# Kernel tuning notes

Hardware: AMD Instinct MI355X
Metric: run time of the kernel (lower is better)

## Reference

```python
import math
import jax, jax.numpy as jnp
import numpy as np

H = 8
C_HIDDEN = 32
C_Q = 256


def setup_inputs() -> dict:
    key = jax.random.key(0)
    ks = jax.random.split(key, 9)
    B, S, Q, K = 1, 128, 256, 256
    q_x = jax.random.normal(ks[0], (B, S, Q, C_Q), dtype=jnp.float32)
    kv_x = jax.random.normal(ks[1], (B, S, K, C_Q), dtype=jnp.float32)
    bias1 = jax.random.normal(ks[2], (B, S, 1, 1, K), dtype=jnp.float32)
    bias2 = jax.random.normal(ks[3], (B, 1, H, Q, K), dtype=jnp.float32)
    scale = 1.0 / math.sqrt(C_Q)
    wq = jax.random.normal(ks[4], (H * C_HIDDEN, C_Q), dtype=jnp.float32) * scale
    wk = jax.random.normal(ks[5], (H * C_HIDDEN, C_Q), dtype=jnp.float32) * scale
    wv = jax.random.normal(ks[6], (H * C_HIDDEN, C_Q), dtype=jnp.float32) * scale
    wg = jax.random.normal(ks[7], (H * C_HIDDEN, C_Q), dtype=jnp.float32) * scale
    wo = jax.random.normal(ks[8], (C_Q, H * C_HIDDEN), dtype=jnp.float32) * scale
    return {"q_x": q_x, "kv_x": kv_x, "bias1": bias1, "bias2": bias2,
            "wq": wq, "wk": wk, "wv": wv, "wg": wg, "wo": wo}


def _split_heads(x):
    # [..., L, H*c] -> [..., H, L, c]
    y = x.reshape(x.shape[:-1] + (H, C_HIDDEN))
    return jnp.moveaxis(y, -2, -3)


def reference(q_x, kv_x, bias1, bias2, wq, wk, wv, wg, wo):
    # QKV projections (no bias), per-head split, scale q by 1/sqrt(c_hidden)
    q = _split_heads(q_x @ wq.T) / math.sqrt(C_HIDDEN)   # [B,S,H,Q,c]
    k = _split_heads(kv_x @ wk.T)                         # [B,S,H,K,c]
    v = _split_heads(kv_x @ wv.T)                         # [B,S,H,K,c]
    # attention logits with additive biases folded in
    a = jnp.einsum('...hqc,...hkc->...hqk', q, k) + bias1 + bias2
    a = jax.nn.softmax(a, axis=-1)
    o = jnp.einsum('...hqk,...hkc->...hqc', a, v)         # [B,S,H,Q,c]
    o = jnp.moveaxis(o, -3, -2)                           # [B,S,Q,H,c]
    # sigmoid gating from query data
    g = jax.nn.sigmoid(q_x @ wg.T)                        # [B,S,Q,H*c]
    g = g.reshape(g.shape[:-1] + (H, C_HIDDEN))
    o = o * g
    o = o.reshape(o.shape[:-2] + (H * C_HIDDEN,))         # flatten heads
    return o @ wo.T                                       # [B,S,Q,C_Q]
```

## Files before the change

kernel.cpp:

```cpp
#include <hip/hip_runtime.h>
#include <math.h>

#define S_DIM 128
#define H_DIM 8
#define M_TOT (S_DIM * 256)

typedef unsigned short ushort_t;
typedef unsigned int   uint32;
typedef __bf16  v8bf  __attribute__((ext_vector_type(8)));
typedef float   v4f   __attribute__((ext_vector_type(4)));

__device__ inline ushort_t f2b(float x) {
    unsigned int u = __float_as_uint(x);
    u += 0x7fffu + ((u >> 16) & 1u);
    return (ushort_t)(u >> 16);
}
__device__ inline float b2f(ushort_t h) {
    return __uint_as_float(((unsigned int)h) << 16);
}

#define GLDS16(gp, lp) __builtin_amdgcn_global_load_lds( \
    (const __attribute__((address_space(1))) void*)(gp), \
    (__attribute__((address_space(3))) void*)(lp), 16, 0, 0)

__global__ __launch_bounds__(256) void split_x(
    const float* __restrict__ xq, const float* __restrict__ xkv,
    ushort_t* __restrict__ hi, ushort_t* __restrict__ lo)
{
    const size_t BUF4 = (size_t)M_TOT * 64;
    const float* src = blockIdx.y ? xkv : xq;
    size_t base = (size_t)blockIdx.y * BUF4;
    int i = blockIdx.x * 256 + threadIdx.x;
    float4 v = ((const float4*)src)[i];
    ushort4 h, l;
    h.x = f2b(v.x); l.x = f2b(v.x - b2f(h.x));
    h.y = f2b(v.y); l.y = f2b(v.y - b2f(h.y));
    h.z = f2b(v.z); l.z = f2b(v.z - b2f(h.z));
    h.w = f2b(v.w); l.w = f2b(v.w - b2f(h.w));
    ((ushort4*)hi)[base + i] = h;
    ((ushort4*)lo)[base + i] = l;
}

__global__ __launch_bounds__(256) void split_w(
    const float* __restrict__ w0, const float* __restrict__ w1,
    const float* __restrict__ w2, const float* __restrict__ w3,
    const float* __restrict__ w4,
    ushort_t* __restrict__ hi, ushort_t* __restrict__ lo)
{
    const float* src;
    switch (blockIdx.y) {
        case 0: src = w0; break; case 1: src = w1; break;
        case 2: src = w2; break; case 3: src = w3; break;
        default: src = w4; break;
    }
    int i = blockIdx.x * 256 + threadIdx.x;
    float4 v = ((const float4*)src)[i];
    ushort4 h, l;
    h.x = f2b(v.x); l.x = f2b(v.x - b2f(h.x));
    h.y = f2b(v.y); l.y = f2b(v.y - b2f(h.y));
    h.z = f2b(v.z); l.z = f2b(v.z - b2f(h.z));
    h.w = f2b(v.w); l.w = f2b(v.w - b2f(h.w));
    size_t base = (size_t)blockIdx.y * 16384;
    ((ushort4*)hi)[base + i] = h;
    ((ushort4*)lo)[base + i] = l;
}


__global__ __launch_bounds__(256) void gemm_proj(
    const ushort_t* __restrict__ Xhi, const ushort_t* __restrict__ Xlo,
    const ushort_t* __restrict__ Whi4, const ushort_t* __restrict__ Wlo4,
    ushort_t* __restrict__ qh, ushort_t* __restrict__ ql,
    ushort_t* __restrict__ kh, ushort_t* __restrict__ kl,
    float* __restrict__ g_out,
    ushort_t* __restrict__ vh,
    float qscale)
{
    __shared__ ushort_t lds[4][128 * 32];

    const int z    = blockIdx.z;
    const int L    = blockIdx.x + 4 * blockIdx.y;
    const int mti  = ((L >> 5) << 3) + (L & 7);
    const int nti  = (L >> 3) & 3;
    const int t    = threadIdx.x;
    const int l    = t & 63;
    const int wv   = t >> 6;
    const int wm   = wv & 1;
    const int wn   = wv >> 1;
    const int idx  = l & 15;
    const int quad = l >> 4;
    const int m0   = mti * 128;
    const int n0   = nti * 128;

    const size_t BUF = (size_t)M_TOT * 256;
    const ushort_t* Ahi = Xhi + (size_t)z * BUF;
    const ushort_t* Alo = Xlo + (size_t)z * BUF;
    const ushort_t* Whi = Whi4 + (size_t)z * 131072;
    const ushort_t* Wlo = Wlo4 + (size_t)z * 131072;
    const float scale = z ? 1.f : qscale;

    const ushort_t* srcs[4] = { Ahi + (size_t)m0 * 256, Alo + (size_t)m0 * 256,
                                Whi + (size_t)n0 * 256, Wlo + (size_t)n0 * 256 };

    v4f acc[4][4];
    #pragma unroll
    for (int i = 0; i < 4; ++i)
        #pragma unroll
        for (int j = 0; j < 4; ++j) acc[i][j] = (v4f){0.f, 0.f, 0.f, 0.f};

    for (int k0 = 0; k0 < 256; k0 += 32) {
        #pragma unroll
        for (int b = 0; b < 4; ++b) {
            #pragma unroll
            for (int i = 0; i < 2; ++i) {
                const int sb   = wv * 128 + i * 64;
                const int slot = sb + l;
                const int row  = slot >> 2;
                const int gseg = ((slot & 3) - (row >> 1)) & 3;
                const ushort_t* g = srcs[b] + (size_t)row * 256 + k0 + gseg * 8;
                GLDS16(g, &lds[b][sb * 8]);
            }
        }
        __builtin_amdgcn_s_waitcnt(0);
        __syncthreads();

        v8bf ah[4], al[4], bh[4], bl[4];
        #pragma unroll
        for (int mt = 0; mt < 4; ++mt) {
            const int r   = wm * 64 + mt * 16 + idx;
            const int off = r * 32 + (((quad + (r >> 1)) & 3) << 3);
            ah[mt] = *(const v8bf*)&lds[0][off];
            al[mt] = *(const v8bf*)&lds[1][off];
        }
        #pragma unroll
        for (int nt = 0; nt < 4; ++nt) {
            const int r   = wn * 64 + nt * 16 + idx;
            const int off = r * 32 + (((quad + (r >> 1)) & 3) << 3);
            bh[nt] = *(const v8bf*)&lds[2][off];
            bl[nt] = *(const v8bf*)&lds[3][off];
        }

        #pragma unroll
        for (int mt = 0; mt < 4; ++mt)
            #pragma unroll
            for (int nt = 0; nt < 4; ++nt) {
                acc[mt][nt] = __builtin_amdgcn_mfma_f32_16x16x32_bf16(ah[mt], bh[nt], acc[mt][nt], 0, 0, 0);
                acc[mt][nt] = __builtin_amdgcn_mfma_f32_16x16x32_bf16(al[mt], bh[nt], acc[mt][nt], 0, 0, 0);
                acc[mt][nt] = __builtin_amdgcn_mfma_f32_16x16x32_bf16(ah[mt], bl[nt], acc[mt][nt], 0, 0, 0);
            }
        __syncthreads();
    }

    ushort_t* dsth = z ? kh : qh;
    ushort_t* dstl = z ? kl : ql;

    #pragma unroll
    for (int mt = 0; mt < 4; ++mt) {
        const int mbase = m0 + wm * 64 + mt * 16 + quad * 4;
        const int s = mbase >> 8, r8 = mbase & 255;
        #pragma unroll
        for (int nt = 0; nt < 4; ++nt) {
            const int gcol = n0 + wn * 64 + nt * 16 + idx;
            if (gcol < 256) {
                const int hh = gcol >> 5, c = gcol & 31;
                const size_t di = (((size_t)(s * 8 + hh) * 256) + r8) * 32 + c;
                #pragma unroll
                for (int r = 0; r < 4; ++r) {
                    const float val = acc[mt][nt][r] * scale;
                    const ushort_t hv = f2b(val);
                    dsth[di + (size_t)r * 32] = hv;
                    dstl[di + (size_t)r * 32] = f2b(val - b2f(hv));
                }
            } else if (z == 0) {
                const int gc = gcol - 256;
                #pragma unroll
                for (int r = 0; r < 4; ++r)
                    g_out[(size_t)(mbase + r) * 256 + gc] = acc[mt][nt][r];
            } else {
                const int gc = gcol - 256, hh = gc >> 5, c = gc & 31;
                ushort4 hv4;
                #pragma unroll
                for (int r = 0; r < 4; ++r)
                    ((ushort_t*)&hv4)[r] = f2b(acc[mt][nt][r]);
                const size_t di = (((size_t)(s * 8 + hh) * 32) + c) * 256 + r8;
                *(ushort4*)&vh[di] = hv4;
            }
        }
    }
}

__global__ __launch_bounds__(256) void gemm_out(
    const ushort_t* __restrict__ Ah, const ushort_t* __restrict__ Whi,
    const ushort_t* __restrict__ Wlo, float* __restrict__ Cf)
{
    __shared__ ushort_t lds[3][128 * 32];

    const int L    = blockIdx.x + 2 * blockIdx.y;
    const int mti  = ((L >> 4) << 3) + (L & 7);
    const int nti  = (L >> 3) & 1;
    const int t    = threadIdx.x;
    const int l    = t & 63;
    const int wv   = t >> 6;
    const int wm   = wv & 1;
    const int wn   = wv >> 1;
    const int idx  = l & 15;
    const int quad = l >> 4;
    const int m0   = mti * 128;
    const int n0   = nti * 128;

    const ushort_t* srcs[3] = { Ah + (size_t)m0 * 256,
                                Whi + (size_t)n0 * 256, Wlo + (size_t)n0 * 256 };

    v4f acc[4][4];
    #pragma unroll
    for (int i = 0; i < 4; ++i)
        #pragma unroll
        for (int j = 0; j < 4; ++j) acc[i][j] = (v4f){0.f, 0.f, 0.f, 0.f};

    for (int k0 = 0; k0 < 256; k0 += 32) {
        #pragma unroll
        for (int b = 0; b < 3; ++b) {
            #pragma unroll
            for (int i = 0; i < 2; ++i) {
                const int sb   = wv * 128 + i * 64;
                const int slot = sb + l;
                const int row  = slot >> 2;
                const int gseg = ((slot & 3) - (row >> 1)) & 3;
                const ushort_t* g = srcs[b] + (size_t)row * 256 + k0 + gseg * 8;
                GLDS16(g, &lds[b][sb * 8]);
            }
        }
        __builtin_amdgcn_s_waitcnt(0);
        __syncthreads();

        v8bf ah[4], bh[4], bl[4];
        #pragma unroll
        for (int mt = 0; mt < 4; ++mt) {
            const int r   = wm * 64 + mt * 16 + idx;
            const int off = r * 32 + (((quad + (r >> 1)) & 3) << 3);
            ah[mt] = *(const v8bf*)&lds[0][off];
        }
        #pragma unroll
        for (int nt = 0; nt < 4; ++nt) {
            const int r   = wn * 64 + nt * 16 + idx;
            const int off = r * 32 + (((quad + (r >> 1)) & 3) << 3);
            bh[nt] = *(const v8bf*)&lds[1][off];
            bl[nt] = *(const v8bf*)&lds[2][off];
        }

        #pragma unroll
        for (int mt = 0; mt < 4; ++mt)
            #pragma unroll
            for (int nt = 0; nt < 4; ++nt) {
                acc[mt][nt] = __builtin_amdgcn_mfma_f32_16x16x32_bf16(ah[mt], bh[nt], acc[mt][nt], 0, 0, 0);
                acc[mt][nt] = __builtin_amdgcn_mfma_f32_16x16x32_bf16(ah[mt], bl[nt], acc[mt][nt], 0, 0, 0);
            }
        __syncthreads();
    }

    #pragma unroll
    for (int mt = 0; mt < 4; ++mt) {
        #pragma unroll
        for (int nt = 0; nt < 4; ++nt) {
            const int gcol = n0 + wn * 64 + nt * 16 + idx;
            #pragma unroll
            for (int r = 0; r < 4; ++r) {
                const int grow = m0 + wm * 64 + mt * 16 + quad * 4 + r;
                Cf[(size_t)grow * 256 + gcol] = acc[mt][nt][r];
            }
        }
    }
}

__global__ __launch_bounds__(256, 2) void attn_mfma(
    const ushort_t* __restrict__ qh, const ushort_t* __restrict__ ql,
    const ushort_t* __restrict__ kh, const ushort_t* __restrict__ kl,
    const ushort_t* __restrict__ vth,
    const float* __restrict__ b1, const float* __restrict__ b2,
    const float* __restrict__ gbuf,
    ushort_t* __restrict__ oh)
{
    __shared__ __align__(16) uint32 pbuf[4][64 * 36];
    __shared__ __align__(16) float  invl[4][64];

    const int sh = blockIdx.x, s = sh >> 3, h = sh & 7;
    const int t = threadIdx.x, l = t & 63, w = t >> 6;
    const int idx = l & 15, quad = l >> 4;

    const size_t shb = (size_t)sh * 8192;
    const ushort_t* qhp = qh + shb;
    const ushort_t* qlp = ql + shb;
    const ushort_t* khp = kh + shb;
    const ushort_t* klp = kl + shb;
    const ushort_t* vhp = vth + shb;
    const float* b1p = b1 + (size_t)s * 256;
    const float* b2p = b2 + (size_t)h * 65536;

    v8bf qfh[4], qfl[4];
    #pragma unroll
    for (int nt = 0; nt < 4; ++nt) {
        const int off = (w * 64 + nt * 16 + idx) * 32 + quad * 8;
        qfh[nt] = *(const v8bf*)(qhp + off);
        qfl[nt] = *(const v8bf*)(qlp + off);
    }

    v4f oacc[4][2];
    #pragma unroll
    for (int mt = 0; mt < 4; ++mt) {
        oacc[mt][0] = (v4f){0.f, 0.f, 0.f, 0.f};
        oacc[mt][1] = (v4f){0.f, 0.f, 0.f, 0.f};
    }
    float lrun[4] = {0.f, 0.f, 0.f, 0.f};

    v8bf kbh[2][4], kbl[2][4];
    #pragma unroll
    for (int at = 0; at < 4; ++at) {
        const int off = (at * 16 + idx) * 32 + quad * 8;
        kbh[0][at] = *(const v8bf*)(khp + off);
        kbl[0][at] = *(const v8bf*)(klp + off);
    }

    #pragma unroll
    for (int c4 = 0; c4 < 4; ++c4) {
        const int ak0 = c4 * 64;
        const int cur = c4 & 1;

        if (c4 < 3) {
            #pragma unroll
            for (int at = 0; at < 4; ++at) {
                const int off = (ak0 + 64 + at * 16 + idx) * 32 + quad * 8;
                kbh[cur ^ 1][at] = *(const v8bf*)(khp + off);
                kbl[cur ^ 1][at] = *(const v8bf*)(klp + off);
            }
        }

        v8bf vfh[2][2];
        #pragma unroll
        for (int n2 = 0; n2 < 2; ++n2)
            #pragma unroll
            for (int kt = 0; kt < 2; ++kt) {
                const int off = (n2 * 16 + idx) * 256 + ak0 + kt * 32 + quad * 8;
                vfh[n2][kt] = *(const v8bf*)(vhp + off);
            }

        v4f sacc[4][4];
        #pragma unroll
        for (int at = 0; at < 4; ++at)
            #pragma unroll
            for (int nt = 0; nt < 4; ++nt)
                sacc[at][nt] = (v4f){0.f, 0.f, 0.f, 0.f};
        __builtin_amdgcn_s_setprio(1);
        #pragma unroll
        for (int at = 0; at < 4; ++at)
            #pragma unroll
            for (int nt = 0; nt < 4; ++nt) {
                sacc[at][nt] = __builtin_amdgcn_mfma_f32_16x16x32_bf16(kbh[cur][at], qfh[nt], sacc[at][nt], 0, 0, 0);
                sacc[at][nt] = __builtin_amdgcn_mfma_f32_16x16x32_bf16(kbl[cur][at], qfh[nt], sacc[at][nt], 0, 0, 0);
                sacc[at][nt] = __builtin_amdgcn_mfma_f32_16x16x32_bf16(kbh[cur][at], qfl[nt], sacc[at][nt], 0, 0, 0);
            }
        __builtin_amdgcn_s_setprio(0);

        v4f b1v[4];
        #pragma unroll
        for (int at = 0; at < 4; ++at)
            b1v[at] = *(const v4f*)(b1p + ak0 + at * 16 + quad * 4);

        #pragma unroll
        for (int at = 0; at < 4; ++at)
            #pragma unroll
            for (int nt = 0; nt < 4; ++nt) {
                const int q = w * 64 + nt * 16 + idx;
                v4f b2v = *(const v4f*)(b2p + (size_t)q * 256 + ak0 + at * 16 + quad * 4);
                float e0 = __expf(b1v[at][0] + b2v[0] + sacc[at][nt][0]);
                float e1 = __expf(b1v[at][1] + b2v[1] + sacc[at][nt][1]);
                float e2 = __expf(b1v[at][2] + b2v[2] + sacc[at][nt][2]);
                float e3 = __expf(b1v[at][3] + b2v[3] + sacc[at][nt][3]);
                lrun[nt] += (e0 + e1) + (e2 + e3);
                uint32 p0 = __builtin_amdgcn_perm(__float_as_uint(e1) + 0x8000u,
                                                  __float_as_uint(e0) + 0x8000u, 0x07060302u);
                uint32 p1 = __builtin_amdgcn_perm(__float_as_uint(e3) + 0x8000u,
                                                  __float_as_uint(e2) + 0x8000u, 0x07060302u);
                const int dw = (nt * 16 + idx) * 36 + at * 8 + quad * 2;
                *(uint2*)&pbuf[w][dw] = make_uint2(p0, p1);
            }

        __builtin_amdgcn_s_setprio(1);
        #pragma unroll
        for (int mt = 0; mt < 4; ++mt)
            #pragma unroll
            for (int kt = 0; kt < 2; ++kt) {
                v8bf pf = *(const v8bf*)&pbuf[w][(mt * 16 + idx) * 36 + kt * 16 + quad * 4];
                #pragma unroll
                for (int n2 = 0; n2 < 2; ++n2)
                    oacc[mt][n2] = __builtin_amdgcn_mfma_f32_16x16x32_bf16(pf, vfh[n2][kt], oacc[mt][n2], 0, 0, 0);
            }
        __builtin_amdgcn_s_setprio(0);
    }

    #pragma unroll
    for (int nt = 0; nt < 4; ++nt) {
        float v = lrun[nt];
        v += __shfl_xor(v, 16, 64);
        v += __shfl_xor(v, 32, 64);
        if (quad == 0) invl[w][nt * 16 + idx] = 1.f / v;
    }

    #pragma unroll
    for (int mt = 0; mt < 4; ++mt) {
        v4f iv = *(const v4f*)&invl[w][mt * 16 + quad * 4];
        #pragma unroll
        for (int n2 = 0; n2 < 2; ++n2) {
            const int c = n2 * 16 + idx;
            #pragma unroll
            for (int r = 0; r < 4; ++r) {
                const int q = w * 64 + mt * 16 + quad * 4 + r;
                const size_t gi = (size_t)(s * 256 + q) * 256 + h * 32 + c;
                const float gv = gbuf[gi];
                const float sig = 1.f / (1.f + __expf(-gv));
                oh[gi] = f2b(oacc[mt][n2][r] * iv[r] * sig);
            }
        }
    }
}

extern "C" void kernel_launch(void* const* d_in, const int* in_sizes, int n_in,
                              void* d_out, int out_size, void* d_ws, size_t ws_size,
                              hipStream_t stream)
{
    const float* q_x   = (const float*)d_in[0];
    const float* kv_x  = (const float*)d_in[1];
    const float* bias1 = (const float*)d_in[2];
    const float* bias2 = (const float*)d_in[3];
    const float* wq    = (const float*)d_in[4];
    const float* wk    = (const float*)d_in[5];
    const float* wv    = (const float*)d_in[6];
    const float* wg    = (const float*)d_in[7];
    const float* wo    = (const float*)d_in[8];
    float* out = (float*)d_out;

    const size_t BUF = (size_t)M_TOT * 256;

    float*    g_buf = (float*)d_ws;
    ushort_t* p     = (ushort_t*)(g_buf + BUF);
    ushort_t* qhb = p;            ushort_t* qlb = qhb + BUF;
    ushort_t* khb = qlb + BUF;    ushort_t* klb = khb + BUF;
    ushort_t* vhb = klb + BUF;
    ushort_t* ohb = vhb + BUF;
    ushort_t* xhb = ohb + BUF;    ushort_t* xlb = xhb + 2 * BUF;
    ushort_t* w_hi = xlb + 2 * BUF;
    ushort_t* w_lo = w_hi + 5 * 65536;

    const float qscale = 0.17677669529663689f;

    split_w<<<dim3(64, 5), 256, 0, stream>>>(wq, wg, wk, wv, wo, w_hi, w_lo);

    split_x<<<dim3(8192, 2), 256, 0, stream>>>(q_x, kv_x, xhb, xlb);

    gemm_proj<<<dim3(4, 256, 2), 256, 0, stream>>>(
        xhb, xlb, w_hi, w_lo, qhb, qlb, khb, klb, g_buf, vhb, qscale);

    attn_mfma<<<S_DIM * H_DIM, 256, 0, stream>>>(
        qhb, qlb, khb, klb, vhb, bias1, bias2, g_buf, ohb);

    gemm_out<<<dim3(2, 256), 256, 0, stream>>>(
        ohb, w_hi + 4 * 65536, w_lo + 4 * 65536, out);
}
```

Measured before the change: 310.5 us.

## Stage K and V tiles through LDS with async global_load_lds double buffering

Before this change, every wave loaded the K high/low and V^T tiles straight from global memory into registers, so the four waves of a block fetched the same data redundantly. Now the block loads each 64-key chunk once into a swizzled, double-buffered LDS staging area with global_load_lds, prefetching the next chunk while computing the current one. Waves then read their fragments from LDS, and a rotated segment layout is meant to avoid bank conflicts. This adds LDS use (about 24KB more), which may reduce occupancy, plus a full waitcnt and barrier on every iteration, and the c4 loop is no longer force-unrolled.

```diff
diff --git a/kernel.cpp b/kernel.cpp
--- a/kernel.cpp
+++ b/kernel.cpp
@@ -279,8 +279,9 @@
     const float* __restrict__ gbuf,
     ushort_t* __restrict__ oh)
 {
-    __shared__ __align__(16) uint32 pbuf[4][64 * 36];
-    __shared__ __align__(16) float  invl[4][64];
+    __shared__ __align__(16) uint32   pbuf[4][64 * 36];
+    __shared__ __align__(16) ushort_t kst[2][3][2048];
+    __shared__ __align__(16) float    invl[4][64];
 
     const int sh = blockIdx.x, s = sh >> 3, h = sh & 7;
     const int t = threadIdx.x, l = t & 63, w = t >> 6;
@@ -295,6 +296,14 @@
     const float* b1p = b1 + (size_t)s * 256;
     const float* b2p = b2 + (size_t)h * 65536;
 
+    const int ksrow = t >> 2;
+    const int ksseg = (( (t & 3) - (ksrow >> 1)) & 3);
+    const int vsrow = t >> 3;
+    const int vsseg = (( (t & 7) - (vsrow >> 1)) & 7);
+    const size_t koff = (size_t)ksrow * 32 + ksseg * 8;
+    const size_t voff = (size_t)vsrow * 256 + vsseg * 8;
+    const int wbase = w * 512;
+
     v8bf qfh[4], qfl[4];
     #pragma unroll
     for (int nt = 0; nt < 4; ++nt) {
@@ -311,36 +320,31 @@
     }
     float lrun[4] = {0.f, 0.f, 0.f, 0.f};
 
-    v8bf kbh[2][4], kbl[2][4];
-    #pragma unroll
-    for (int at = 0; at < 4; ++at) {
-        const int off = (at * 16 + idx) * 32 + quad * 8;
-        kbh[0][at] = *(const v8bf*)(khp + off);
-        kbl[0][at] = *(const v8bf*)(klp + off);
-    }
-
-    #pragma unroll
+    GLDS16(khp + koff, &kst[0][0][wbase]);
+    GLDS16(klp + koff, &kst[0][1][wbase]);
+    GLDS16(vhp + voff, &kst[0][2][wbase]);
+    __builtin_amdgcn_s_waitcnt(0);
+    __syncthreads();
+
     for (int c4 = 0; c4 < 4; ++c4) {
         const int ak0 = c4 * 64;
         const int cur = c4 & 1;
 
         if (c4 < 3) {
-            #pragma unroll
-            for (int at = 0; at < 4; ++at) {
-                const int off = (ak0 + 64 + at * 16 + idx) * 32 + quad * 8;
-                kbh[cur ^ 1][at] = *(const v8bf*)(khp + off);
-                kbl[cur ^ 1][at] = *(const v8bf*)(klp + off);
-            }
-        }
-
-        v8bf vfh[2][2];
-        #pragma unroll
-        for (int n2 = 0; n2 < 2; ++n2)
-            #pragma unroll
-            for (int kt = 0; kt < 2; ++kt) {
-                const int off = (n2 * 16 + idx) * 256 + ak0 + kt * 32 + quad * 8;
-                vfh[n2][kt] = *(const v8bf*)(vhp + off);
-            }
+            const size_t nb = (size_t)(ak0 + 64) * 32;
+            GLDS16(khp + nb + koff, &kst[cur ^ 1][0][wbase]);
+            GLDS16(klp + nb + koff, &kst[cur ^ 1][1][wbase]);
+            GLDS16(vhp + (ak0 + 64) + voff, &kst[cur ^ 1][2][wbase]);
+        }
+
+        v8bf kfh[4], kfl[4];
+        #pragma unroll
+        for (int at = 0; at < 4; ++at) {
+            const int row = at * 16 + idx;
+            const int off = row * 32 + (((quad + (row >> 1)) & 3) << 3);
+            kfh[at] = *(const v8bf*)&kst[cur][0][off];
+            kfl[at] = *(const v8bf*)&kst[cur][1][off];
+        }
 
         v4f sacc[4][4];
         #pragma unroll
@@ -353,11 +357,21 @@
         for (int at = 0; at < 4; ++at)
             #pragma unroll
             for (int nt = 0; nt < 4; ++nt) {
-                sacc[at][nt] = __builtin_amdgcn_mfma_f32_16x16x32_bf16(kbh[cur][at], qfh[nt], sacc[at][nt], 0, 0, 0);
-                sacc[at][nt] = __builtin_amdgcn_mfma_f32_16x16x32_bf16(kbl[cur][at], qfh[nt], sacc[at][nt], 0, 0, 0);
-                sacc[at][nt] = __builtin_amdgcn_mfma_f32_16x16x32_bf16(kbh[cur][at], qfl[nt], sacc[at][nt], 0, 0, 0);
+                sacc[at][nt] = __builtin_amdgcn_mfma_f32_16x16x32_bf16(kfh[at], qfh[nt], sacc[at][nt], 0, 0, 0);
+                sacc[at][nt] = __builtin_amdgcn_mfma_f32_16x16x32_bf16(kfl[at], qfh[nt], sacc[at][nt], 0, 0, 0);
+                sacc[at][nt] = __builtin_amdgcn_mfma_f32_16x16x32_bf16(kfh[at], qfl[nt], sacc[at][nt], 0, 0, 0);
             }
         __builtin_amdgcn_s_setprio(0);
+
+        v8bf vfh[2][2];
+        #pragma unroll
+        for (int n2 = 0; n2 < 2; ++n2)
+            #pragma unroll
+            for (int kt = 0; kt < 2; ++kt) {
+                const int c  = n2 * 16 + idx;
+                const int sp = ((kt * 4 + quad) + (c >> 1)) & 7;
+                vfh[n2][kt] = *(const v8bf*)&kst[cur][2][c * 64 + sp * 8];
+            }
 
         v4f b1v[4];
         #pragma unroll
@@ -394,6 +408,9 @@
                     oacc[mt][n2] = __builtin_amdgcn_mfma_f32_16x16x32_bf16(pf, vfh[n2][kt], oacc[mt][n2], 0, 0, 0);
             }
         __builtin_amdgcn_s_setprio(0);
+
+        __builtin_amdgcn_s_waitcnt(0);
+        __syncthreads();
     }
 
     #pragma unroll
```

After: 269.2 us. -13.3%, faster.
